# Kernel optimization log

Measured on AMD Instinct MI355X. Metric: run time of the kernel, lower is better.

Reference implementation:

```python
import jax, jax.numpy as jnp
import numpy as np

LN2 = float(np.log(2.0))
EPS = 1e-5

def layer_norm(x, scale, bias):
    mu = jnp.mean(x, axis=-1, keepdims=True)
    var = jnp.var(x, axis=-1, keepdims=True)
    return (x - mu) * jax.lax.rsqrt(var + EPS) * scale + bias

def shifted_softplus(x):
    return jax.nn.softplus(x) - LN2

def setup_inputs() -> dict:
    key = jax.random.key(0)
    N, E, H = 50000, 800000, 128
    ks = jax.random.split(key, 12)
    s = 0.05
    inp = {
        'h_V': jax.random.normal(ks[0], (N, H), jnp.float32),
        'h_E': jax.random.normal(ks[1], (E, H), jnp.float32),
        'edge_index': jax.random.randint(ks[2], (2, E), 0, N, jnp.int64),
        # attention weights (stored [in, out])
        'W_Q': jax.random.normal(ks[3], (H, H), jnp.float32) * s,
        'W_K': jax.random.normal(ks[4], (2 * H, H), jnp.float32) * s,
        'W_V': jax.random.normal(ks[5], (2 * H, H), jnp.float32) * s,
        'W_O': jax.random.normal(ks[6], (H, H), jnp.float32) * s,
        # layernorms
        'ln1_scale': jnp.ones((H,), jnp.float32),
        'ln1_bias': jnp.zeros((H,), jnp.float32),
        'ln2_scale': jnp.ones((H,), jnp.float32),
        'ln2_bias': jnp.zeros((H,), jnp.float32),
        # FFN (num_ff == num_hidden in TransformerLayer)
        'W_in': jax.random.normal(ks[7], (H, H), jnp.float32) * s,
        'b_in': jnp.zeros((H,), jnp.float32),
        'W_out': jax.random.normal(ks[8], (H, H), jnp.float32) * s,
        'b_out': jnp.zeros((H,), jnp.float32),
    }
    return inp

def reference(h_V, h_E, edge_index, W_Q, W_K, W_V, W_O,
              ln1_scale, ln1_bias, ln2_scale, ln2_bias,
              W_in, b_in, W_out, b_out):
    N, H = h_V.shape
    E = h_E.shape[0]
    n_heads = 4
    d = H // n_heads
    row, col = edge_index[0], edge_index[1]

    # --- attention block ---
    y = layer_norm(h_V, ln1_scale, ln1_bias)
    hv_col = y[col]                                  # [E, H] gather
    he = jnp.concatenate([h_E, hv_col], axis=-1)     # [E, 2H]
    Q = (y @ W_Q).reshape(N, n_heads, d)             # [N, h, d]
    K = (he @ W_K).reshape(E, n_heads, d)            # [E, h, d]
    V = (he @ W_V).reshape(E, n_heads, d)            # [E, h, d]
    logits = jnp.sum(Q[row] * K, axis=-1)            # [E, h]

    # scatter softmax over destination node `row`
    m = jax.ops.segment_max(logits, row, num_segments=N)      # [N, h]
    m = jnp.where(jnp.isfinite(m), m, 0.0)
    ex = jnp.exp(logits - m[row])                              # [E, h]
    denom = jax.ops.segment_sum(ex, row, num_segments=N)      # [N, h]
    alpha = ex / denom[row] / jnp.sqrt(jnp.float32(d))         # faithful: scale AFTER softmax

    msg = alpha[..., None] * V                                 # [E, h, d]
    aggr = jax.ops.segment_sum(msg, row, num_segments=N)      # [N, h, d]
    attn_out = shifted_softplus(aggr.reshape(N, H)) @ W_O      # [N, H]

    h_V = h_V + attn_out  # dropout is identity (eval)

    # --- FFN block ---
    y = layer_norm(h_V, ln2_scale, ln2_bias)
    y = jax.nn.relu(y @ W_in + b_in) @ W_out + b_out
    h_V = h_V + y
    return h_V
```

## Files before the change

kernel.cpp:

```cpp
#include <hip/hip_runtime.h>


typedef __bf16 bf16x8 __attribute__((ext_vector_type(8)));
typedef float f32x4 __attribute__((ext_vector_type(4)));
typedef unsigned short u16x8 __attribute__((ext_vector_type(8)));

#define DEV static __device__ __forceinline__
#define ET 32

DEV unsigned short f2b(float f){
  union { float f; unsigned u; } v; v.f = f;
  unsigned r = (v.u + 0x7FFFu + ((v.u >> 16) & 1u)) >> 16;
  return (unsigned short)r;
}
DEV float b2f(unsigned short h){
  union { unsigned u; float f; } v; v.u = ((unsigned)h) << 16; return v.f;
}
DEV f32x4 mfma16(bf16x8 a, bf16x8 b, f32x4 c){
  return __builtin_amdgcn_mfma_f32_16x16x32_bf16(a, b, c, 0, 0, 0);
}
DEV u16x8 pack8(float4 a, float4 b){
  u16x8 p;
  p[0]=f2b(a.x); p[1]=f2b(a.y); p[2]=f2b(a.z); p[3]=f2b(a.w);
  p[4]=f2b(b.x); p[5]=f2b(b.y); p[6]=f2b(b.z); p[7]=f2b(b.w);
  return p;
}
DEV float sspf(float x){
  return fmaxf(x, 0.f) + log1pf(expf(-fabsf(x))) - 0.69314718055994531f;
}
DEV int idx64probe(const int* __restrict__ ei){
  return (ei[1] | ei[3] | ei[5] | ei[7] | ei[9]) == 0;
}
DEV int ld_row(const int* __restrict__ ei, long eg, long E, int is64, int N){
  int v = is64 ? ei[2*eg] : ei[eg];
  return min(max(v, 0), N - 1);
}
DEV int ld_col(const int* __restrict__ ei, long eg, long E, int is64, int N){
  int v = is64 ? ei[2*(E + eg)] : ei[E + eg];
  return min(max(v, 0), N - 1);
}
DEV unsigned swz(unsigned byteoff, unsigned row){
  return byteoff ^ ((row & 7u) << 4);
}
DEV void gload16(const void* g, void* l){
  __builtin_amdgcn_global_load_lds((const __attribute__((address_space(1))) void*)g,
                                   (__attribute__((address_space(3))) void*)l, 16, 0, 0);
}
DEV void bar_lds(){
  asm volatile("s_waitcnt lgkmcnt(0)" ::: "memory");
  __builtin_amdgcn_s_barrier();
}

DEV void mma128(const unsigned short* At, const unsigned short* __restrict__ WT,
                int t, f32x4 (&acc)[4][4]){
  const int l = t & 63;
  const int wm = (t >> 7) & 1, wn = (t >> 6) & 1;
#pragma unroll
  for (int m = 0; m < 4; ++m)
#pragma unroll
    for (int n = 0; n < 4; ++n)
      acc[m][n] = f32x4{0.f, 0.f, 0.f, 0.f};
#pragma unroll
  for (int kk = 0; kk < 4; ++kk){
    bf16x8 a[4], b[4];
#pragma unroll
    for (int m = 0; m < 4; ++m){
      int row = wm*64 + m*16 + (l & 15);
      a[m] = *(const bf16x8*)((const char*)At +
              swz((unsigned)(row*256 + kk*64 + ((l >> 4) & 3)*16), (unsigned)row));
    }
#pragma unroll
    for (int n = 0; n < 4; ++n){
      int col = wn*64 + n*16 + (l & 15);
      b[n] = *(const bf16x8*)(WT + col*128 + kk*32 + ((l >> 4) & 3)*8);
    }
#pragma unroll
    for (int m = 0; m < 4; ++m)
#pragma unroll
      for (int n = 0; n < 4; ++n)
        acc[m][n] = mfma16(a[m], b[n], acc[m][n]);
  }
}

DEV void mma32(const unsigned short* Ab, const unsigned short* __restrict__ WT,
               int t, f32x4 (&acc)[4]){
  const int l = t & 63, wid = t >> 6, wm = wid >> 1, wn = wid & 1;
#pragma unroll
  for (int n = 0; n < 4; ++n) acc[n] = f32x4{0.f, 0.f, 0.f, 0.f};
#pragma unroll
  for (int kk = 0; kk < 4; ++kk){
    int row = wm*16 + (l & 15);
    bf16x8 a = *(const bf16x8*)((const char*)Ab +
        swz((unsigned)(row*256 + kk*64 + ((l >> 4) & 3)*16), (unsigned)row));
#pragma unroll
    for (int n = 0; n < 4; ++n){
      int col = wn*64 + n*16 + (l & 15);
      bf16x8 b = *(const bf16x8*)(WT + col*128 + kk*32 + ((l >> 4) & 3)*8);
      acc[n] = mfma16(a, b, acc[n]);
    }
  }
}
DEV void store_acc32(unsigned short* Kt, const f32x4 (&acc)[4], int t){
  const int l = t & 63, wid = t >> 6, wm = wid >> 1, wn = wid & 1;
#pragma unroll
  for (int n = 0; n < 4; ++n)
#pragma unroll
    for (int reg = 0; reg < 4; ++reg){
      int er = wm*16 + ((l >> 4) & 3)*4 + reg;
      int col = wn*64 + n*16 + (l & 15);
      *(unsigned short*)((char*)Kt + swz((unsigned)(er*256 + col*2), (unsigned)er))
          = f2b(acc[n][reg]);
    }
}

__global__ void k_zero(float4* __restrict__ p, long n){
  long i = (long)blockIdx.x * blockDim.x + threadIdx.x;
  const long st = (long)gridDim.x * blockDim.x;
  const float4 z = {0.f, 0.f, 0.f, 0.f};
  for (; i < n; i += st) p[i] = z;
}

__global__ void k_wprep(const float* __restrict__ WQ, const float* __restrict__ WK,
                        const float* __restrict__ WV, const float* __restrict__ WO,
                        const float* __restrict__ Wi, const float* __restrict__ Wo2,
                        unsigned short* WQT, unsigned short* WKtT, unsigned short* WKbT,
                        unsigned short* WVtT, unsigned short* WVbT, unsigned short* WOT,
                        unsigned short* WinT, unsigned short* WouT){
  int id = blockIdx.x * 256 + threadIdx.x;
  int n = id >> 7, k = id & 127;
  int d = n * 128 + k;
  WQT[d]  = f2b(WQ[k*128 + n]);
  WKtT[d] = f2b(WK[k*128 + n]);
  WKbT[d] = f2b(WK[(k+128)*128 + n]);
  WVtT[d] = f2b(WV[k*128 + n]);
  WVbT[d] = f2b(WV[(k+128)*128 + n]);
  WOT[d]  = f2b(WO[k*128 + n]);
  WinT[d] = f2b(Wi[k*128 + n]);
  WouT[d] = f2b(Wo2[k*128 + n]);
}

__global__ void k_hist(const int* __restrict__ ei, int* __restrict__ cnt, long E, int N){
  const int is64 = idx64probe(ei);
  long i = (long)blockIdx.x * blockDim.x + threadIdx.x;
  const long st = (long)gridDim.x * blockDim.x;
  for (; i < E; i += st) atomicAdd(&cnt[ld_row(ei, i, E, is64, N)], 1);
}

DEV int wave_incl_scan(int v, int lane){
#pragma unroll
  for (int ofs = 1; ofs < 64; ofs <<= 1){
    int u = __shfl_up(v, ofs, 64);
    if (lane >= ofs) v += u;
  }
  return v;
}

__global__ __launch_bounds__(1024) void k_scan(const int* __restrict__ cnt,
                                               int* __restrict__ cursor,
                                               int4* __restrict__ edata,
                                               long E, int N){
  __shared__ int wsum[16], woff[16];
  const int t = threadIdx.x, lane = t & 63, w = t >> 6;
  const int C = (N + 1023) / 1024;
  const int base = t * C;
  int s = 0;
  for (int j = 0; j < C; ++j) if (base + j < N) s += cnt[base + j];
  int incl = wave_incl_scan(s, lane);
  if (lane == 63) wsum[w] = incl;
  __syncthreads();
  if (t == 0){
    int run = 0;
#pragma unroll
    for (int i = 0; i < 16; ++i){ woff[i] = run; run += wsum[i]; }
  }
  __syncthreads();
  int run = woff[w] + incl - s;
  for (int j = 0; j < C; ++j)
    if (base + j < N){ cursor[base + j] = run; run += cnt[base + j]; }
  if (t < 37){
    long gi = (t == 0) ? 0 : (E + t);
    edata[gi] = make_int4(0, -2, 0, 0);
  }
}

__global__ void k_scatter(const int* __restrict__ ei, int* __restrict__ cursor,
                          int4* __restrict__ edata, long E, int N){
  const int is64 = idx64probe(ei);
  long i = (long)blockIdx.x * blockDim.x + threadIdx.x;
  const long st = (long)gridDim.x * blockDim.x;
  for (; i < E; i += st){
    int r = ld_row(ei, i, E, is64, N);
    int c = ld_col(ei, i, E, is64, N);
    int pos = atomicAdd(&cursor[r], 1);
    edata[1 + (long)pos] = make_int4((int)i, r, c, 0);
  }
}

__global__ __launch_bounds__(256) void k_nodeprep(
    const float* __restrict__ hV, const float* __restrict__ l1s, const float* __restrict__ l1b,
    const unsigned short* __restrict__ WQT, const unsigned short* __restrict__ WKbT,
    const unsigned short* __restrict__ WVbT,
    unsigned short* __restrict__ Qbf, unsigned short* __restrict__ YKbf,
    unsigned short* __restrict__ YVbf, int N){
  __shared__ unsigned short At[128*128];
  __shared__ float ps[256], pss[256];
  __shared__ float scs[128], bis[128];
  const int t = threadIdx.x;
  if (t < 128){ scs[t] = l1s[t]; bis[t] = l1b[t]; }
  const int r0 = blockIdx.x * 128;
  const int rl = t & 127, hf = t >> 7;
  const int r = r0 + rl;
  const float4* xp = (const float4*)(hV + (size_t)r*128 + hf*64);
  float s = 0.f, ss = 0.f;
  if (r < N){
#pragma unroll
    for (int i = 0; i < 16; ++i){
      float4 v = xp[i];
      s  += (v.x + v.y) + (v.z + v.w);
      ss += (v.x*v.x + v.y*v.y) + (v.z*v.z + v.w*v.w);
    }
  }
  ps[t] = s; pss[t] = ss;
  __syncthreads();
  const float mu  = (ps[t] + ps[t ^ 128]) * 0.0078125f;
  const float var = (pss[t] + pss[t ^ 128]) * 0.0078125f - mu*mu;
  const float rs  = rsqrtf(var + 1e-5f);
#pragma unroll
  for (int i = 0; i < 8; ++i){
    const int c = hf*64 + i*8;
    u16x8 p = {0,0,0,0,0,0,0,0};
    if (r < N){
      float4 v0 = xp[2*i], v1 = xp[2*i+1];
      p[0] = f2b((v0.x - mu)*rs*scs[c+0] + bis[c+0]);
      p[1] = f2b((v0.y - mu)*rs*scs[c+1] + bis[c+1]);
      p[2] = f2b((v0.z - mu)*rs*scs[c+2] + bis[c+2]);
      p[3] = f2b((v0.w - mu)*rs*scs[c+3] + bis[c+3]);
      p[4] = f2b((v1.x - mu)*rs*scs[c+4] + bis[c+4]);
      p[5] = f2b((v1.y - mu)*rs*scs[c+5] + bis[c+5]);
      p[6] = f2b((v1.z - mu)*rs*scs[c+6] + bis[c+6]);
      p[7] = f2b((v1.w - mu)*rs*scs[c+7] + bis[c+7]);
    }
    *(u16x8*)((char*)At + swz((unsigned)(rl*256 + c*2), (unsigned)rl)) = p;
  }
  __syncthreads();
  const int l = t & 63, wm = (t >> 7) & 1, wn = (t >> 6) & 1;
  f32x4 acc[4][4];
  for (int g = 0; g < 3; ++g){
    const unsigned short* WT = (g == 0) ? WQT : (g == 1) ? WKbT : WVbT;
    unsigned short* O = (g == 0) ? Qbf : (g == 1) ? YKbf : YVbf;
    mma128(At, WT, t, acc);
#pragma unroll
    for (int m = 0; m < 4; ++m)
#pragma unroll
      for (int reg = 0; reg < 4; ++reg){
        int row = wm*64 + m*16 + ((l >> 4) & 3)*4 + reg;
        int gr = r0 + row;
        if (gr < N){
#pragma unroll
          for (int n = 0; n < 4; ++n){
            int col = wn*64 + n*16 + (l & 15);
            O[(size_t)gr*128 + col] = f2b(acc[m][n][reg]);
          }
        }
      }
  }
}

__global__ __launch_bounds__(256, 3) void k_edge(
    const float* __restrict__ hE,
    const unsigned short* __restrict__ WKtT, const unsigned short* __restrict__ WVtT,
    const unsigned short* __restrict__ Qbf, const unsigned short* __restrict__ YKbf,
    const unsigned short* __restrict__ YVbf,
    const int4* __restrict__ edata,
    float* __restrict__ num, float* __restrict__ den,
    long E, long NT){
  __shared__ float4 stage[2][ET*32];
  __shared__ unsigned short Ab[ET*128];
  __shared__ unsigned short Kt[ET*128];
  __shared__ float aS[ET][4];
  __shared__ int4 idxb[3][36];

  const int t = threadIdx.x, l = t & 63, wid = t >> 6;
  const long b0 = blockIdx.x, G = gridDim.x;
  const long ntloc = (b0 < NT) ? ((NT - 1 - b0) / G + 1) : 0;

  auto tileof = [&](long i) -> long {
    long tt = b0 + i * G; return (tt < NT) ? tt : (NT - 1);
  };
  auto issue_idx = [&](long i, int slot){
    long tt = tileof(i);
    if (l < 9)
      gload16((const void*)(edata + tt*ET + (wid*9 + l)), (void*)&idxb[slot][wid*9]);
  };
  auto issue_pf = [&](long i, int buf){
    const int slot = (int)(i % 3);
#pragma unroll
    for (int k = 0; k < 4; ++k){
      int U = (wid*4 + k)*64 + l;
      int row = U >> 5, u = U & 31;
      int pe = idxb[slot][1 + row].x;
      pe = min(max(pe, 0), (int)(E - 1));
      int j = u ^ (row & 7);
      gload16((const void*)(hE + (size_t)pe*128 + j*4),
              (void*)&stage[buf][(wid*4 + k)*64]);
    }
  };

  issue_idx(0, 0);
  issue_idx(1, 1);
  asm volatile("s_waitcnt vmcnt(1)" ::: "memory");
  __builtin_amdgcn_sched_barrier(0);
  __builtin_amdgcn_s_barrier();
  issue_pf(0, 0);
  int p = 0;

  for (long it = 0; it < ntloc; ++it){
    const int slot = (int)(it % 3);
    asm volatile("s_waitcnt vmcnt(0) lgkmcnt(0)" ::: "memory");
    __builtin_amdgcn_sched_barrier(0);
    __builtin_amdgcn_s_barrier();
    {
      const int row = t >> 3, s = t & 7;
      float4 f[4];
#pragma unroll
      for (int k = 0; k < 4; ++k)
        f[k] = stage[p][row*32 + ((s*4 + k) ^ (row & 7))];
      *(u16x8*)((char*)Ab + swz((unsigned)(row*256 + s*32), (unsigned)row)) = pack8(f[0], f[1]);
      *(u16x8*)((char*)Ab + swz((unsigned)(row*256 + s*32 + 16), (unsigned)row)) = pack8(f[2], f[3]);
    }
    bar_lds();
    { f32x4 acc[4]; mma32(Ab, WKtT, t, acc); store_acc32(Kt, acc, t); }
    bar_lds();
    {
      const int e = t >> 3, s = t & 7;
      int4 ed = idxb[slot][1 + e];
      int r = ed.y;
      int ra = max(r, 0), ca = max(ed.z, 0);
      const u16x8* qp  = (const u16x8*)(Qbf  + (size_t)ra*128 + s*16);
      const u16x8* ykp = (const u16x8*)(YKbf + (size_t)ca*128 + s*16);
      float pl = 0.f;
#pragma unroll
      for (int k = 0; k < 2; ++k){
        u16x8 q = qp[k], yk = ykp[k];
        u16x8 kv = *(const u16x8*)((const char*)Kt +
            swz((unsigned)(e*256 + s*32 + k*16), (unsigned)e));
#pragma unroll
        for (int j = 0; j < 8; ++j) pl += b2f(q[j]) * (b2f(kv[j]) + b2f(yk[j]));
      }
      float full = pl + __shfl_xor(pl, 1);
      if (!(s & 1)) aS[e][s >> 1] = (r >= 0) ? expf(full) : 0.f;
    }
    bar_lds();
    { f32x4 acc[4]; mma32(Ab, WVtT, t, acc); store_acc32(Kt, acc, t); }
    bar_lds();
    {
      const int e = t >> 3, s = t & 7;
      int ca = max(idxb[slot][1 + e].z, 0);
      const u16x8* src = (const u16x8*)(YVbf + (size_t)ca*128 + s*16);
#pragma unroll
      for (int k = 0; k < 2; ++k){
        u16x8* pp = (u16x8*)((char*)Kt + swz((unsigned)(e*256 + s*32 + k*16), (unsigned)e));
        u16x8 a = *pp, b = src[k], o;
#pragma unroll
        for (int j = 0; j < 8; ++j) o[j] = f2b(b2f(a[j]) + b2f(b[j]));
        *pp = o;
      }
    }
    bar_lds();
    issue_idx(it + 2, (int)((it + 2) % 3));
    issue_pf(it + 1, p ^ 1);
    {
      const int c = t & 127, half = t >> 7, hh = c >> 5;
      const int eb = half * 16;
      auto rowAt = [&](int x) -> int { return idxb[slot][1 + x].y; };
      auto flush = [&](int rr, int rsx, int rex, float av, float ad){
        if (rr < 0) return;
        bool own = (rowAt(rsx - 1) != rr) && (rowAt(rex) != rr);
        float* np = num + (size_t)rr*128 + c;
        if (own) *np = av; else atomicAdd(np, av);
        if (c < 4){
          float* dp = den + (size_t)rr*4 + c;
          if (own) *dp = ad; else atomicAdd(dp, ad);
        }
      };
      float accv = 0.f, accd = 0.f;
      int cur = rowAt(eb), rs = eb;
#pragma unroll
      for (int e = eb; e < eb + 16; ++e){
        int r = rowAt(e);
        if (r != cur){ flush(cur, rs, e, accv, accd); cur = r; rs = e; accv = 0.f; accd = 0.f; }
        float a = aS[e][hh];
        accv += a * b2f(*(const unsigned short*)((const char*)Kt +
                  swz((unsigned)(e*256 + c*2), (unsigned)e)));
        if (c < 4) accd += aS[e][c];
      }
      flush(cur, rs, eb + 16, accv, accd);
    }
    p ^= 1;
  }
  asm volatile("s_waitcnt vmcnt(0) lgkmcnt(0)" ::: "memory");
  __builtin_amdgcn_s_barrier();
}

__global__ __launch_bounds__(256, 2) void k_post(
    const float* __restrict__ hV, const float* __restrict__ num,
    const float* __restrict__ den,
    const unsigned short* __restrict__ WOT, const unsigned short* __restrict__ WinT,
    const unsigned short* __restrict__ WouT,
    const float* __restrict__ l2s, const float* __restrict__ l2b,
    const float* __restrict__ bin, const float* __restrict__ bou,
    float* __restrict__ out, int N){
  __shared__ unsigned short At[128*128];
  __shared__ float ps[128][2], pq[128][2];
  __shared__ float scs[128], bis[128], binS[128], bouS[128];
  const int t = threadIdx.x;
  if (t < 128){ scs[t] = l2s[t]; bis[t] = l2b[t]; binS[t] = bin[t]; bouS[t] = bou[t]; }
  const int r0 = blockIdx.x * 128;
  const int rl = t & 127, hf = t >> 7;
  const int r = r0 + rl;
  const float inv = 0.17677669529663687f;
  float i0 = 0.f, i1 = 0.f;
  if (r < N){
    float d0 = den[(size_t)r*4 + 2*hf], d1 = den[(size_t)r*4 + 2*hf + 1];
    i0 = (d0 > 0.f) ? inv / d0 : 0.f;
    i1 = (d1 > 0.f) ? inv / d1 : 0.f;
  }
  const float4* ap = (const float4*)(num + (size_t)r*128 + hf*64);
#pragma unroll
  for (int i = 0; i < 8; ++i){
    u16x8 p = {0,0,0,0,0,0,0,0};
    if (r < N){
      float sc = (i < 4) ? i0 : i1;
      float4 v0 = ap[2*i], v1 = ap[2*i+1];
      p[0]=f2b(sspf(v0.x*sc)); p[1]=f2b(sspf(v0.y*sc)); p[2]=f2b(sspf(v0.z*sc)); p[3]=f2b(sspf(v0.w*sc));
      p[4]=f2b(sspf(v1.x*sc)); p[5]=f2b(sspf(v1.y*sc)); p[6]=f2b(sspf(v1.z*sc)); p[7]=f2b(sspf(v1.w*sc));
    }
    *(u16x8*)((char*)At + swz((unsigned)(rl*256 + hf*128 + i*16), (unsigned)rl)) = p;
  }
  __syncthreads();
  const int l = t & 63, wm = (t >> 7) & 1, wn = (t >> 6) & 1;
  f32x4 acc[4][4];
  mma128(At, WOT, t, acc);
  float h1[4][4][4];
#pragma unroll
  for (int m = 0; m < 4; ++m)
#pragma unroll
    for (int reg = 0; reg < 4; ++reg){
      int er = wm*64 + m*16 + ((l >> 4) & 3)*4 + reg;
      int gr = r0 + er;
#pragma unroll
      for (int n = 0; n < 4; ++n){
        int col = wn*64 + n*16 + (l & 15);
        h1[m][n][reg] = acc[m][n][reg] + ((gr < N) ? hV[(size_t)gr*128 + col] : 0.f);
      }
    }
#pragma unroll
  for (int m = 0; m < 4; ++m)
#pragma unroll
    for (int reg = 0; reg < 4; ++reg){
      float s = 0.f, q = 0.f;
#pragma unroll
      for (int n = 0; n < 4; ++n){ float v = h1[m][n][reg]; s += v; q += v*v; }
#pragma unroll
      for (int o = 1; o < 16; o <<= 1){ s += __shfl_xor(s, o); q += __shfl_xor(q, o); }
      if ((l & 15) == 0){
        int er = wm*64 + m*16 + ((l >> 4) & 3)*4 + reg;
        ps[er][wn] = s; pq[er][wn] = q;
      }
    }
  __syncthreads();
#pragma unroll
  for (int m = 0; m < 4; ++m)
#pragma unroll
    for (int reg = 0; reg < 4; ++reg){
      int er = wm*64 + m*16 + ((l >> 4) & 3)*4 + reg;
      float mu  = (ps[er][0] + ps[er][1]) * 0.0078125f;
      float var = (pq[er][0] + pq[er][1]) * 0.0078125f - mu*mu;
      float rsv = rsqrtf(var + 1e-5f);
#pragma unroll
      for (int n = 0; n < 4; ++n){
        int col = wn*64 + n*16 + (l & 15);
        float yv = (h1[m][n][reg] - mu)*rsv*scs[col] + bis[col];
        *(unsigned short*)((char*)At + swz((unsigned)(er*256 + col*2), (unsigned)er)) = f2b(yv);
      }
    }
  __syncthreads();
  mma128(At, WinT, t, acc);
  __syncthreads();
#pragma unroll
  for (int m = 0; m < 4; ++m)
#pragma unroll
    for (int reg = 0; reg < 4; ++reg){
      int er = wm*64 + m*16 + ((l >> 4) & 3)*4 + reg;
#pragma unroll
      for (int n = 0; n < 4; ++n){
        int col = wn*64 + n*16 + (l & 15);
        float v = acc[m][n][reg] + binS[col];
        *(unsigned short*)((char*)At + swz((unsigned)(er*256 + col*2), (unsigned)er))
            = f2b(fmaxf(v, 0.f));
      }
    }
  __syncthreads();
  mma128(At, WouT, t, acc);
#pragma unroll
  for (int m = 0; m < 4; ++m)
#pragma unroll
    for (int reg = 0; reg < 4; ++reg){
      int er = wm*64 + m*16 + ((l >> 4) & 3)*4 + reg;
      int gr = r0 + er;
      if (gr < N){
#pragma unroll
        for (int n = 0; n < 4; ++n){
          int col = wn*64 + n*16 + (l & 15);
          out[(size_t)gr*128 + col] = acc[m][n][reg] + bouS[col] + h1[m][n][reg];
        }
      }
    }
}

extern "C" void kernel_launch(void* const* d_in, const int* in_sizes, int n_in,
                              void* d_out, int out_size, void* d_ws, size_t ws_size,
                              hipStream_t stream)
{
  const float* hV  = (const float*)d_in[0];
  const float* hE  = (const float*)d_in[1];
  const int*   ei  = (const int*)d_in[2];
  const float* WQ  = (const float*)d_in[3];
  const float* WK  = (const float*)d_in[4];
  const float* WV  = (const float*)d_in[5];
  const float* WO  = (const float*)d_in[6];
  const float* l1s = (const float*)d_in[7];
  const float* l1b = (const float*)d_in[8];
  const float* l2s = (const float*)d_in[9];
  const float* l2b = (const float*)d_in[10];
  const float* Wi  = (const float*)d_in[11];
  const float* bi  = (const float*)d_in[12];
  const float* Wo2 = (const float*)d_in[13];
  const float* bo  = (const float*)d_in[14];
  float* out = (float*)d_out;

  const int  N = in_sizes[0] / 128;
  const long E = (long)in_sizes[1] / 128;
  const long NT = (E + ET - 1) / ET;

  char* ws = (char*)d_ws;
  size_t off = 0;
  auto alloc = [&](size_t b){ size_t o = off; off += (b + 255) & ~(size_t)255; return o; };
  const size_t WB = 128*128*sizeof(unsigned short);
  size_t oWQT = alloc(WB), oWKtT = alloc(WB), oWKbT = alloc(WB);
  size_t oWVtT = alloc(WB), oWVbT = alloc(WB), oWOT = alloc(WB);
  size_t oWinT = alloc(WB), oWouT = alloc(WB);
  size_t oQ    = alloc((size_t)N*128*2);
  size_t oYK   = alloc((size_t)N*128*2);
  size_t oYV   = alloc((size_t)N*128*2);
  size_t oED   = alloc((size_t)(E + 38)*16);
  size_t oCUR  = alloc((size_t)N*4);
  size_t oCNT  = alloc((size_t)N*4);
  size_t oDEN  = alloc((size_t)N*4*4);
  size_t oNUM  = alloc((size_t)N*128*4);
  size_t zero_bytes = (oNUM + (size_t)N*128*4) - oCNT;

  unsigned short* WQT  = (unsigned short*)(ws + oWQT);
  unsigned short* WKtT = (unsigned short*)(ws + oWKtT);
  unsigned short* WKbT = (unsigned short*)(ws + oWKbT);
  unsigned short* WVtT = (unsigned short*)(ws + oWVtT);
  unsigned short* WVbT = (unsigned short*)(ws + oWVbT);
  unsigned short* WOT  = (unsigned short*)(ws + oWOT);
  unsigned short* WinT = (unsigned short*)(ws + oWinT);
  unsigned short* WouT = (unsigned short*)(ws + oWouT);
  unsigned short* Qbf  = (unsigned short*)(ws + oQ);
  unsigned short* YKbf = (unsigned short*)(ws + oYK);
  unsigned short* YVbf = (unsigned short*)(ws + oYV);
  int4* edata  = (int4*)(ws + oED);
  int* cursor  = (int*)(ws + oCUR);
  int* cnt     = (int*)(ws + oCNT);
  float* den   = (float*)(ws + oDEN);
  float* num   = (float*)(ws + oNUM);

  const int nbN = (N + 127) / 128;
  const int nbe = (int)((E + 255) / 256);
  const int gE  = (int)((NT < 768) ? NT : 768);

  k_zero<<<2048, 256, 0, stream>>>((float4*)(ws + oCNT), (long)(zero_bytes / 16));
  k_wprep<<<64, 256, 0, stream>>>(WQ, WK, WV, WO, Wi, Wo2,
                                  WQT, WKtT, WKbT, WVtT, WVbT, WOT, WinT, WouT);
  k_nodeprep<<<nbN, 256, 0, stream>>>(hV, l1s, l1b, WQT, WKbT, WVbT, Qbf, YKbf, YVbf, N);
  k_hist<<<nbe, 256, 0, stream>>>(ei, cnt, E, N);
  k_scan<<<1, 1024, 0, stream>>>(cnt, cursor, edata, E, N);
  k_scatter<<<nbe, 256, 0, stream>>>(ei, cursor, edata, E, N);
  k_edge<<<gE, 256, 0, stream>>>(hE, WKtT, WVtT, Qbf, YKbf, YVbf,
                                 edata, num, den, E, NT);
  k_post<<<nbN, 256, 0, stream>>>(hV, num, den, WOT, WinT, WouT,
                                  l2s, l2b, bi, bo, out, N);
}
```

Baseline: 921.4 us.

## Replace LDS async staging in edge kernel with register double-buffered prefetch

The edge kernel drops the global_load_lds staging buffers and index ring in shared memory. Instead, each thread prefetches its edge indices and h_E row into registers two tiles ahead, ping-ponging between two register sets. Row ids for segment detection go into a small LDS array. The freed LDS allows occupancy to rise from 3 to 4 blocks per CU and the grid grows to 1024 blocks, at the cost of more register pressure and loads that are now synchronous from the register file's point of view.

```diff
diff --git a/kernel.cpp b/kernel.cpp
--- a/kernel.cpp
+++ b/kernel.cpp
@@ -41,10 +41,6 @@
 }
 DEV unsigned swz(unsigned byteoff, unsigned row){
   return byteoff ^ ((row & 7u) << 4);
-}
-DEV void gload16(const void* g, void* l){
-  __builtin_amdgcn_global_load_lds((const __attribute__((address_space(1))) void*)g,
-                                   (__attribute__((address_space(3))) void*)l, 16, 0, 0);
 }
 DEV void bar_lds(){
   asm volatile("s_waitcnt lgkmcnt(0)" ::: "memory");
@@ -266,7 +262,7 @@
   }
 }
 
-__global__ __launch_bounds__(256, 3) void k_edge(
+__global__ __launch_bounds__(256, 4) void k_edge(
     const float* __restrict__ hE,
     const unsigned short* __restrict__ WKtT, const unsigned short* __restrict__ WVtT,
     const unsigned short* __restrict__ Qbf, const unsigned short* __restrict__ YKbf,
@@ -274,68 +270,46 @@
     const int4* __restrict__ edata,
     float* __restrict__ num, float* __restrict__ den,
     long E, long NT){
-  __shared__ float4 stage[2][ET*32];
   __shared__ unsigned short Ab[ET*128];
   __shared__ unsigned short Kt[ET*128];
   __shared__ float aS[ET][4];
-  __shared__ int4 idxb[3][36];
-
-  const int t = threadIdx.x, l = t & 63, wid = t >> 6;
+  __shared__ int rowsT[ET + 2];
+
+  const int t = threadIdx.x;
+  const int er = t >> 3, s = t & 7;
   const long b0 = blockIdx.x, G = gridDim.x;
   const long ntloc = (b0 < NT) ? ((NT - 1 - b0) / G + 1) : 0;
+  if (ntloc == 0) return;
 
   auto tileof = [&](long i) -> long {
     long tt = b0 + i * G; return (tt < NT) ? tt : (NT - 1);
   };
-  auto issue_idx = [&](long i, int slot){
-    long tt = tileof(i);
-    if (l < 9)
-      gload16((const void*)(edata + tt*ET + (wid*9 + l)), (void*)&idxb[slot][wid*9]);
+  auto ldED = [&](long i) -> int4 {
+    return edata[1 + tileof(i)*ET + er];
   };
-  auto issue_pf = [&](long i, int buf){
-    const int slot = (int)(i % 3);
-#pragma unroll
-    for (int k = 0; k < 4; ++k){
-      int U = (wid*4 + k)*64 + l;
-      int row = U >> 5, u = U & 31;
-      int pe = idxb[slot][1 + row].x;
-      pe = min(max(pe, 0), (int)(E - 1));
-      int j = u ^ (row & 7);
-      gload16((const void*)(hE + (size_t)pe*128 + j*4),
-              (void*)&stage[buf][(wid*4 + k)*64]);
-    }
+  auto ldHE = [&](const int4& ed, float4 (&R)[4]){
+    long pe = ed.x; pe = (pe < 0) ? 0 : (pe >= E ? E - 1 : pe);
+    const float4* src = (const float4*)(hE + (size_t)pe*128 + s*16);
+#pragma unroll
+    for (int k = 0; k < 4; ++k) R[k] = src[k];
   };
 
-  issue_idx(0, 0);
-  issue_idx(1, 1);
-  asm volatile("s_waitcnt vmcnt(1)" ::: "memory");
-  __builtin_amdgcn_sched_barrier(0);
-  __builtin_amdgcn_s_barrier();
-  issue_pf(0, 0);
-  int p = 0;
-
-  for (long it = 0; it < ntloc; ++it){
-    const int slot = (int)(it % 3);
-    asm volatile("s_waitcnt vmcnt(0) lgkmcnt(0)" ::: "memory");
-    __builtin_amdgcn_sched_barrier(0);
-    __builtin_amdgcn_s_barrier();
-    {
-      const int row = t >> 3, s = t & 7;
-      float4 f[4];
-#pragma unroll
-      for (int k = 0; k < 4; ++k)
-        f[k] = stage[p][row*32 + ((s*4 + k) ^ (row & 7))];
-      *(u16x8*)((char*)Ab + swz((unsigned)(row*256 + s*32), (unsigned)row)) = pack8(f[0], f[1]);
-      *(u16x8*)((char*)Ab + swz((unsigned)(row*256 + s*32 + 16), (unsigned)row)) = pack8(f[2], f[3]);
-    }
+  int4 edA, edB;
+  float4 A[4], B[4];
+  edA = ldED(0); ldHE(edA, A);
+  edB = ldED(1); ldHE(edB, B);
+
+  auto proc = [&](float4 (&R)[4], int4& ed, long it){
+    const int rowC = ed.y, colC = ed.z;
+    ed = ldED(it + 2);
+    *(u16x8*)((char*)Ab + swz((unsigned)(er*256 + s*32),      (unsigned)er)) = pack8(R[0], R[1]);
+    *(u16x8*)((char*)Ab + swz((unsigned)(er*256 + s*32 + 16), (unsigned)er)) = pack8(R[2], R[3]);
+    ldHE(ed, R);
     bar_lds();
     { f32x4 acc[4]; mma32(Ab, WKtT, t, acc); store_acc32(Kt, acc, t); }
     bar_lds();
     {
-      const int e = t >> 3, s = t & 7;
-      int4 ed = idxb[slot][1 + e];
-      int r = ed.y;
-      int ra = max(r, 0), ca = max(ed.z, 0);
+      int ra = max(rowC, 0), ca = max(colC, 0);
       const u16x8* qp  = (const u16x8*)(Qbf  + (size_t)ra*128 + s*16);
       const u16x8* ykp = (const u16x8*)(YKbf + (size_t)ca*128 + s*16);
       float pl = 0.f;
@@ -343,23 +317,28 @@
       for (int k = 0; k < 2; ++k){
         u16x8 q = qp[k], yk = ykp[k];
         u16x8 kv = *(const u16x8*)((const char*)Kt +
-            swz((unsigned)(e*256 + s*32 + k*16), (unsigned)e));
+            swz((unsigned)(er*256 + s*32 + k*16), (unsigned)er));
 #pragma unroll
         for (int j = 0; j < 8; ++j) pl += b2f(q[j]) * (b2f(kv[j]) + b2f(yk[j]));
       }
       float full = pl + __shfl_xor(pl, 1);
-      if (!(s & 1)) aS[e][s >> 1] = (r >= 0) ? expf(full) : 0.f;
+      if (!(s & 1)) aS[er][s >> 1] = (rowC >= 0) ? expf(full) : 0.f;
+      if (s == 0) rowsT[1 + er] = rowC;
+      if (t == 0){
+        long base = tileof(it)*ET;
+        rowsT[0]      = edata[base].y;
+        rowsT[1 + ET] = edata[1 + base + ET].y;
+      }
     }
     bar_lds();
     { f32x4 acc[4]; mma32(Ab, WVtT, t, acc); store_acc32(Kt, acc, t); }
     bar_lds();
     {
-      const int e = t >> 3, s = t & 7;
-      int ca = max(idxb[slot][1 + e].z, 0);
+      int ca = max(colC, 0);
       const u16x8* src = (const u16x8*)(YVbf + (size_t)ca*128 + s*16);
 #pragma unroll
       for (int k = 0; k < 2; ++k){
-        u16x8* pp = (u16x8*)((char*)Kt + swz((unsigned)(e*256 + s*32 + k*16), (unsigned)e));
+        u16x8* pp = (u16x8*)((char*)Kt + swz((unsigned)(er*256 + s*32 + k*16), (unsigned)er));
         u16x8 a = *pp, b = src[k], o;
 #pragma unroll
         for (int j = 0; j < 8; ++j) o[j] = f2b(b2f(a[j]) + b2f(b[j]));
@@ -367,12 +346,10 @@
       }
     }
     bar_lds();
-    issue_idx(it + 2, (int)((it + 2) % 3));
-    issue_pf(it + 1, p ^ 1);
     {
       const int c = t & 127, half = t >> 7, hh = c >> 5;
       const int eb = half * 16;
-      auto rowAt = [&](int x) -> int { return idxb[slot][1 + x].y; };
+      auto rowAt = [&](int x) -> int { return rowsT[1 + x]; };
       auto flush = [&](int rr, int rsx, int rex, float av, float ad){
         if (rr < 0) return;
         bool own = (rowAt(rsx - 1) != rr) && (rowAt(rex) != rr);
@@ -396,10 +373,11 @@
       }
       flush(cur, rs, eb + 16, accv, accd);
     }
-    p ^= 1;
-  }
-  asm volatile("s_waitcnt vmcnt(0) lgkmcnt(0)" ::: "memory");
-  __builtin_amdgcn_s_barrier();
+  };
+
+  long it = 0;
+  for (; it + 1 < ntloc; it += 2){ proc(A, edA, it); proc(B, edB, it + 1); }
+  if (it < ntloc) proc(A, edA, it);
 }
 
 __global__ __launch_bounds__(256, 2) void k_post(
@@ -579,7 +557,7 @@
 
   const int nbN = (N + 127) / 128;
   const int nbe = (int)((E + 255) / 256);
-  const int gE  = (int)((NT < 768) ? NT : 768);
+  const int gE  = (int)((NT < 1024) ? NT : 1024);
 
   k_zero<<<2048, 256, 0, stream>>>((float4*)(ws + oCNT), (long)(zero_bytes / 16));
   k_wprep<<<64, 256, 0, stream>>>(WQ, WK, WV, WO, Wi, Wo2,
```

Result: slower. 1.083 ms (+17.6%).
